# Kernel tuning notes

Measured on AMD Instinct MI355X. Metric: run time of the kernel, lower is better.

## Reference

```python
import jax, jax.numpy as jnp
import numpy as np

VOCAB, EMB, HID = 32000, 512, 1024

def setup_inputs() -> dict:
    key = jax.random.key(0)
    k1, k2, k3, k4, k5, k6 = jax.random.split(key, 6)
    s_e = 1.0 / np.sqrt(EMB)
    s_h = 1.0 / np.sqrt(HID)
    return {
        "x": jax.random.randint(k1, (32, 512), 0, VOCAB, dtype=jnp.int64),
        "emb_table": jax.random.normal(k2, (VOCAB, EMB), dtype=jnp.float32),
        "W_ih": jax.random.uniform(k3, (4 * HID, EMB), jnp.float32, -s_h, s_h),
        "W_hh": jax.random.uniform(k4, (4 * HID, HID), jnp.float32, -s_h, s_h),
        "b_ih": jax.random.uniform(k5, (4 * HID,), jnp.float32, -s_h, s_h),
        "b_hh": jax.random.uniform(k6, (4 * HID,), jnp.float32, -s_h, s_h),
    }

def _lstm(embedded, W_ih, W_hh, b_ih, b_hh):
    # embedded: [B, T, E]; gates order (PyTorch): i, f, g, o
    B = embedded.shape[0]
    H = W_hh.shape[1]
    # Precompute input projections for all timesteps: [B, T, 4H]
    x_proj = jnp.einsum('bte,ge->btg', embedded, W_ih) + b_ih + b_hh

    def step(carry, xt):
        h, c = carry
        gates = xt + h @ W_hh.T  # [B, 4H]
        i, f, g, o = jnp.split(gates, 4, axis=-1)
        i = jax.nn.sigmoid(i)
        f = jax.nn.sigmoid(f)
        g = jnp.tanh(g)
        o = jax.nn.sigmoid(o)
        c = f * c + i * g
        h = o * jnp.tanh(c)
        return (h, c), h

    h0 = jnp.zeros((B, H), embedded.dtype)
    c0 = jnp.zeros((B, H), embedded.dtype)
    (h_f, c_f), hs = jax.lax.scan(step, (h0, c0), jnp.swapaxes(x_proj, 0, 1))
    return jnp.swapaxes(hs, 0, 1), h_f, c_f

def reference(x, emb_table, W_ih, W_hh, b_ih, b_hh):
    embedded = emb_table[x]  # [B, T, E]
    encoder_outputs, state_h, state_c = _lstm(embedded, W_ih, W_hh, b_ih, b_hh)
    return encoder_outputs, state_h, state_c
```

## Files before the change

### kernel.cpp

```cpp
#include <hip/hip_runtime.h>

#define Bb 32
#define Tt 512
#define Ee 512
#define Hh 1024

typedef __attribute__((ext_vector_type(8))) short bf16x8;
typedef __attribute__((ext_vector_type(4))) float f32x4;
typedef __attribute__((ext_vector_type(4))) unsigned u32x4;
typedef unsigned long long u64;

#define SEN 0x7FC0u

__device__ __forceinline__ unsigned short f2bf(float f) {
  unsigned int u = __float_as_uint(f);
  u = (u + 0x7fffu + ((u >> 16) & 1u)) >> 16;
  return (unsigned short)u;
}
__device__ __forceinline__ float bf2f(unsigned short s) {
  return __uint_as_float(((unsigned int)s) << 16);
}
__device__ __forceinline__ float sigmoidf_(float x) {
  x = fminf(fmaxf(x, -30.f), 30.f);
  return 1.f / (1.f + __expf(-x));
}
__device__ __forceinline__ float tanh_fast(float x) {
  float xx = fminf(fmaxf(x, -15.f), 15.f);
  float e = __expf(2.f * xx);
  return (e - 1.f) / (e + 1.f);
}
__device__ __forceinline__ bool frag_bad(u32x4 v) {
  return ((v[0] & 0xFFFFu) == SEN) | ((v[1] & 0xFFFFu) == SEN) |
         ((v[2] & 0xFFFFu) == SEN) | ((v[3] & 0xFFFFu) == SEN);
}

__global__ void gather_kernel(const int* __restrict__ x,
                              const float* __restrict__ emb,
                              unsigned short* __restrict__ emb_hi,
                              unsigned short* __restrict__ emb_lo,
                              unsigned short* __restrict__ hbuf) {
  long long gid = (long long)blockIdx.x * blockDim.x + threadIdx.x;
  long long stride = (long long)gridDim.x * blockDim.x;
  for (long long i = gid; i < 8192; i += stride)
    ((ushort4*)hbuf)[i] = make_ushort4(0, 0, 0, 0);
  for (long long i = 8192 + gid; i < 4194304; i += stride)
    ((ushort4*)hbuf)[i] =
        make_ushort4((unsigned short)SEN, (unsigned short)SEN,
                     (unsigned short)SEN, (unsigned short)SEN);
  long long n4 = (long long)Bb * Tt * Ee / 4;
  for (long long i = gid; i < n4; i += stride) {
    long long bt = i >> 7;
    int e4 = (int)(i & 127);
    int row = x[bt];
    row = min(max(row, 0), 31999);
    float4 v = ((const float4*)(emb + (long long)row * Ee))[e4];
    ushort4 hv, lv;
    hv.x = f2bf(v.x); lv.x = f2bf(v.x - bf2f(hv.x));
    hv.y = f2bf(v.y); lv.y = f2bf(v.y - bf2f(hv.y));
    hv.z = f2bf(v.z); lv.z = f2bf(v.z - bf2f(hv.z));
    hv.w = f2bf(v.w); lv.w = f2bf(v.w - bf2f(hv.w));
    ((ushort4*)emb_hi)[i] = hv;
    ((ushort4*)emb_lo)[i] = lv;
  }
}

__global__ __launch_bounds__(256, 1)
void lstm_kernel(const unsigned short* __restrict__ emb_hi,
                 const unsigned short* __restrict__ emb_lo,
                 unsigned short* __restrict__ hbuf,
                 const float* __restrict__ W_ih,
                 const float* __restrict__ W_hh,
                 const float* __restrict__ b_ih,
                 const float* __restrict__ b_hh,
                 float* __restrict__ out) {
  __shared__ unsigned short sWih_hi[16 * 512];
  __shared__ unsigned short sWih_lo[16 * 512];
  __shared__ unsigned short sWhh_hi[16 * 1024];
  __shared__ unsigned short sWhh_lo[16 * 1024];
  __shared__ float sAcc[2][4][2][16][17];
  __shared__ float sBias[16];
  __shared__ float sC[32][4];

  const int tid = threadIdx.x;
  const int lane = tid & 63;
  const int wv = tid >> 6;
  const int wg = blockIdx.x;
  const int j0 = (wg & 7) * 128 + (wg >> 3) * 4;

  for (int idx = tid; idx < 16 * 64; idx += 256) {
    int c = idx >> 6, kc8 = idx & 63;
    int grow = (c >> 2) * Hh + j0 + (c & 3);
    const float* src = W_ih + (long long)grow * Ee + kc8 * 8;
    int us = (c * 512 + kc8 * 8) ^ ((c & 7) << 3);
#pragma unroll
    for (int j = 0; j < 8; j++) {
      float f = src[j];
      unsigned short h = f2bf(f);
      sWih_hi[us + j] = h;
      sWih_lo[us + j] = f2bf(f - bf2f(h));
    }
  }
  for (int idx = tid; idx < 16 * 128; idx += 256) {
    int c = idx >> 7, kc8 = idx & 127;
    int grow = (c >> 2) * Hh + j0 + (c & 3);
    const float* src = W_hh + (long long)grow * Hh + kc8 * 8;
    int us = (c * 1024 + kc8 * 8) ^ ((c & 7) << 3);
#pragma unroll
    for (int j = 0; j < 8; j++) {
      float f = src[j];
      unsigned short h = f2bf(f);
      sWhh_hi[us + j] = h;
      sWhh_lo[us + j] = f2bf(f - bf2f(h));
    }
  }
  if (tid < 16) {
    int grow = (tid >> 2) * Hh + j0 + (tid & 3);
    sBias[tid] = b_ih[grow] + b_hh[grow];
  }
  if (tid < 128) sC[tid >> 2][tid & 3] = 0.f;
  __syncthreads();

  const int r16 = lane & 15;
  const int kg = (lane >> 4) * 8;
  const int col = lane & 15;
  const int xr = (col & 7) << 3;

  float h_last = 0.f, c_last = 0.f;

  for (int t = 0; t < Tt; t++) {
    __builtin_amdgcn_sched_barrier(0);

    const u32x4* hb4 = (const u32x4*)(hbuf + (u64)t * 32768);
    const u64* hb8 = (const u64*)(hbuf + (u64)t * 32768);
    u32x4 hA[8], hB[8];
    int iA[8], iB[8];
#pragma unroll
    for (int q = 0; q < 8; q++) {
      int kc = wv + q * 4;
      iA[q] = (r16 * Hh + kc * 32 + kg) >> 3;
      iB[q] = ((16 + r16) * Hh + kc * 32 + kg) >> 3;
      hA[q] = hb4[iA[q]];
      hB[q] = hb4[iB[q]];
    }

    f32x4 acc[2][3];
#pragma unroll
    for (int mt = 0; mt < 2; mt++)
#pragma unroll
      for (int cb = 0; cb < 3; cb++)
        acc[mt][cb] = (f32x4){0.f, 0.f, 0.f, 0.f};
#pragma unroll
    for (int q = 0; q < 4; q++) {
      int kc = wv + q * 4;
      int bo = (col * 512 + kc * 32 + kg) ^ xr;
      bf16x8 bH = *(const bf16x8*)(sWih_hi + bo);
      bf16x8 bL = *(const bf16x8*)(sWih_lo + bo);
#pragma unroll
      for (int mt = 0; mt < 2; mt++) {
        int rb = mt * 16 + r16;
        int ai = (rb * Tt + t) * Ee + kc * 32 + kg;
        bf16x8 aH = *(const bf16x8*)(emb_hi + ai);
        bf16x8 aL = *(const bf16x8*)(emb_lo + ai);
        acc[mt][0] = __builtin_amdgcn_mfma_f32_16x16x32_bf16(aH, bH, acc[mt][0], 0, 0, 0);
        acc[mt][1] = __builtin_amdgcn_mfma_f32_16x16x32_bf16(aH, bL, acc[mt][1], 0, 0, 0);
        acc[mt][2] = __builtin_amdgcn_mfma_f32_16x16x32_bf16(aL, bH, acc[mt][2], 0, 0, 0);
      }
    }

#pragma unroll
    for (int q = 0; q < 8; q++) {
      int kc = wv + q * 4;
      u32x4 va = hA[q], vb = hB[q];
      bool bad = frag_bad(va) | frag_bad(vb);
      while (__any(bad)) {
        if (bad) {
          u64 a0 = __hip_atomic_load(hb8 + iA[q] * 2, __ATOMIC_RELAXED,
                                     __HIP_MEMORY_SCOPE_AGENT);
          u64 a1 = __hip_atomic_load(hb8 + iA[q] * 2 + 1, __ATOMIC_RELAXED,
                                     __HIP_MEMORY_SCOPE_AGENT);
          u64 b0 = __hip_atomic_load(hb8 + iB[q] * 2, __ATOMIC_RELAXED,
                                     __HIP_MEMORY_SCOPE_AGENT);
          u64 b1 = __hip_atomic_load(hb8 + iB[q] * 2 + 1, __ATOMIC_RELAXED,
                                     __HIP_MEMORY_SCOPE_AGENT);
          va[0] = (unsigned)a0; va[1] = (unsigned)(a0 >> 32);
          va[2] = (unsigned)a1; va[3] = (unsigned)(a1 >> 32);
          vb[0] = (unsigned)b0; vb[1] = (unsigned)(b0 >> 32);
          vb[2] = (unsigned)b1; vb[3] = (unsigned)(b1 >> 32);
        }
        bad = frag_bad(va) | frag_bad(vb);
      }
      union { u32x4 u; bf16x8 v; } ua, ub;
      ua.u = va; ub.u = vb;
      int bo = (col * 1024 + kc * 32 + kg) ^ xr;
      bf16x8 bH = *(const bf16x8*)(sWhh_hi + bo);
      bf16x8 bL = *(const bf16x8*)(sWhh_lo + bo);
      acc[0][0] = __builtin_amdgcn_mfma_f32_16x16x32_bf16(ua.v, bH, acc[0][0], 0, 0, 0);
      acc[0][1] = __builtin_amdgcn_mfma_f32_16x16x32_bf16(ua.v, bL, acc[0][1], 0, 0, 0);
      acc[1][0] = __builtin_amdgcn_mfma_f32_16x16x32_bf16(ub.v, bH, acc[1][0], 0, 0, 0);
      acc[1][1] = __builtin_amdgcn_mfma_f32_16x16x32_bf16(ub.v, bL, acc[1][1], 0, 0, 0);
    }

#pragma unroll
    for (int mt = 0; mt < 2; mt++) {
      f32x4 tot = acc[mt][0] + acc[mt][1] + acc[mt][2];
#pragma unroll
      for (int r = 0; r < 4; r++)
        sAcc[t & 1][wv][mt][(lane >> 4) * 4 + r][col] = tot[r];
    }
    __syncthreads();

    if (tid < 128) {
      int b = tid >> 2, du = tid & 3;
      int mt = b >> 4, rr = b & 15;
      float g0 = sBias[0 * 4 + du], g1 = sBias[1 * 4 + du];
      float g2 = sBias[2 * 4 + du], g3 = sBias[3 * 4 + du];
#pragma unroll
      for (int w = 0; w < 4; w++) {
        g0 += sAcc[t & 1][w][mt][rr][0 * 4 + du];
        g1 += sAcc[t & 1][w][mt][rr][1 * 4 + du];
        g2 += sAcc[t & 1][w][mt][rr][2 * 4 + du];
        g3 += sAcc[t & 1][w][mt][rr][3 * 4 + du];
      }
      float ig = sigmoidf_(g0);
      float fg = sigmoidf_(g1);
      float gg = tanh_fast(g2);
      float og = sigmoidf_(g3);
      float cn = fg * sC[b][du] + ig * gg;
      sC[b][du] = cn;
      float hn = og * tanh_fast(cn);
      h_last = hn; c_last = cn;

      unsigned pack = (unsigned)f2bf(hn);
      unsigned other = __shfl_xor(pack, 1, 64);
      if (t + 1 < Tt && (du & 1) == 0) {
        unsigned w = (pack & 0xffffu) | (other << 16);
        unsigned* nb32 = (unsigned*)(hbuf + (u64)(t + 1) * 32768);
        __hip_atomic_store(nb32 + ((b * 1024 + j0 + du) >> 1), w,
                           __ATOMIC_RELAXED, __HIP_MEMORY_SCOPE_AGENT);
      }
      out[((long long)b * Tt + t) * Hh + j0 + du] = hn;
    }
  }

  if (tid < 128) {
    int b = tid >> 2, du = tid & 3;
    int hj = j0 + du;
    out[16777216LL + b * Hh + hj] = h_last;
    out[16777216LL + 32768 + b * Hh + hj] = c_last;
  }
}

extern "C" void kernel_launch(void* const* d_in, const int* in_sizes, int n_in,
                              void* d_out, int out_size, void* d_ws, size_t ws_size,
                              hipStream_t stream) {
  const int* x      = (const int*)d_in[0];
  const float* emb  = (const float*)d_in[1];
  const float* W_ih = (const float*)d_in[2];
  const float* W_hh = (const float*)d_in[3];
  const float* b_ih = (const float*)d_in[4];
  const float* b_hh = (const float*)d_in[5];
  float* out = (float*)d_out;

  unsigned short* emb_hi = (unsigned short*)d_ws;
  unsigned short* emb_lo = emb_hi + 8388608;
  unsigned short* hbuf   = emb_lo + 8388608;

  hipLaunchKernelGGL(gather_kernel, dim3(2048), dim3(256), 0, stream,
                     x, emb, emb_hi, emb_lo, hbuf);

  void* args[] = { (void*)&emb_hi, (void*)&emb_lo, (void*)&hbuf,
                   (void*)&W_ih, (void*)&W_hh, (void*)&b_ih, (void*)&b_hh,
                   (void*)&out };
  hipError_t e = hipLaunchCooperativeKernel((void*)lstm_kernel, dim3(256),
                                            dim3(256), args, 0, stream);
  if (e != hipSuccess) {
    hipLaunchKernelGGL(lstm_kernel, dim3(256), dim3(256), 0, stream,
                       emb_hi, emb_lo, hbuf, W_ih, W_hh, b_ih, b_hh, out);
  }
}
```

Baseline: 3.440 ms.

## Drop split-bf16 compensation and halve workgroups with 8 hidden units each

Removes the hi/lo bf16 split of the weights and embeddings, so each product is a single bf16 MFMA instead of three. Each workgroup now owns 8 hidden units (32 gate rows) instead of 4, which halves the grid to 128 blocks. Waves are re-split into two row tiles times two K halves, and all 256 threads run the cell update. This cuts MFMA count, LDS traffic and the number of blocks synchronizing through the h buffer, at the cost of lower precision in the gate pre-activations.

```diff
diff --git a/kernel.cpp b/kernel.cpp
--- a/kernel.cpp
+++ b/kernel.cpp
@@ -17,9 +17,6 @@
   u = (u + 0x7fffu + ((u >> 16) & 1u)) >> 16;
   return (unsigned short)u;
 }
-__device__ __forceinline__ float bf2f(unsigned short s) {
-  return __uint_as_float(((unsigned int)s) << 16);
-}
 __device__ __forceinline__ float sigmoidf_(float x) {
   x = fminf(fmaxf(x, -30.f), 30.f);
   return 1.f / (1.f + __expf(-x));
@@ -37,7 +34,6 @@
 __global__ void gather_kernel(const int* __restrict__ x,
                               const float* __restrict__ emb,
                               unsigned short* __restrict__ emb_hi,
-                              unsigned short* __restrict__ emb_lo,
                               unsigned short* __restrict__ hbuf) {
   long long gid = (long long)blockIdx.x * blockDim.x + threadIdx.x;
   long long stride = (long long)gridDim.x * blockDim.x;
@@ -54,76 +50,62 @@
     int row = x[bt];
     row = min(max(row, 0), 31999);
     float4 v = ((const float4*)(emb + (long long)row * Ee))[e4];
-    ushort4 hv, lv;
-    hv.x = f2bf(v.x); lv.x = f2bf(v.x - bf2f(hv.x));
-    hv.y = f2bf(v.y); lv.y = f2bf(v.y - bf2f(hv.y));
-    hv.z = f2bf(v.z); lv.z = f2bf(v.z - bf2f(hv.z));
-    hv.w = f2bf(v.w); lv.w = f2bf(v.w - bf2f(hv.w));
+    ushort4 hv;
+    hv.x = f2bf(v.x); hv.y = f2bf(v.y);
+    hv.z = f2bf(v.z); hv.w = f2bf(v.w);
     ((ushort4*)emb_hi)[i] = hv;
-    ((ushort4*)emb_lo)[i] = lv;
   }
 }
 
 __global__ __launch_bounds__(256, 1)
 void lstm_kernel(const unsigned short* __restrict__ emb_hi,
-                 const unsigned short* __restrict__ emb_lo,
                  unsigned short* __restrict__ hbuf,
                  const float* __restrict__ W_ih,
                  const float* __restrict__ W_hh,
                  const float* __restrict__ b_ih,
                  const float* __restrict__ b_hh,
                  float* __restrict__ out) {
-  __shared__ unsigned short sWih_hi[16 * 512];
-  __shared__ unsigned short sWih_lo[16 * 512];
-  __shared__ unsigned short sWhh_hi[16 * 1024];
-  __shared__ unsigned short sWhh_lo[16 * 1024];
-  __shared__ float sAcc[2][4][2][16][17];
-  __shared__ float sBias[16];
-  __shared__ float sC[32][4];
+  __shared__ unsigned short sWih[32 * 512];
+  __shared__ unsigned short sWhh[32 * 1024];
+  __shared__ float sAcc[2][2][2][2][16][17];
+  __shared__ float sBias[32];
+  __shared__ float sC[32][8];
 
   const int tid = threadIdx.x;
   const int lane = tid & 63;
   const int wv = tid >> 6;
   const int wg = blockIdx.x;
-  const int j0 = (wg & 7) * 128 + (wg >> 3) * 4;
-
-  for (int idx = tid; idx < 16 * 64; idx += 256) {
-    int c = idx >> 6, kc8 = idx & 63;
-    int grow = (c >> 2) * Hh + j0 + (c & 3);
-    const float* src = W_ih + (long long)grow * Ee + kc8 * 8;
-    int us = (c * 512 + kc8 * 8) ^ ((c & 7) << 3);
-#pragma unroll
-    for (int j = 0; j < 8; j++) {
-      float f = src[j];
-      unsigned short h = f2bf(f);
-      sWih_hi[us + j] = h;
-      sWih_lo[us + j] = f2bf(f - bf2f(h));
-    }
-  }
-  for (int idx = tid; idx < 16 * 128; idx += 256) {
-    int c = idx >> 7, kc8 = idx & 127;
-    int grow = (c >> 2) * Hh + j0 + (c & 3);
-    const float* src = W_hh + (long long)grow * Hh + kc8 * 8;
-    int us = (c * 1024 + kc8 * 8) ^ ((c & 7) << 3);
-#pragma unroll
-    for (int j = 0; j < 8; j++) {
-      float f = src[j];
-      unsigned short h = f2bf(f);
-      sWhh_hi[us + j] = h;
-      sWhh_lo[us + j] = f2bf(f - bf2f(h));
-    }
-  }
-  if (tid < 16) {
-    int grow = (tid >> 2) * Hh + j0 + (tid & 3);
+  const int j0 = (wg & 7) * 128 + (wg >> 3) * 8;
+
+  for (int idx = tid; idx < 32 * 64; idx += 256) {
+    int c = idx >> 6, k8 = idx & 63;
+    int grow = (c >> 3) * Hh + j0 + (c & 7);
+    const float* src = W_ih + (long long)grow * Ee + k8 * 8;
+    int us = (c * 512 + k8 * 8) ^ ((c & 7) << 3);
+#pragma unroll
+    for (int j = 0; j < 8; j++) sWih[us + j] = f2bf(src[j]);
+  }
+  for (int idx = tid; idx < 32 * 128; idx += 256) {
+    int c = idx >> 7, k8 = idx & 127;
+    int grow = (c >> 3) * Hh + j0 + (c & 7);
+    const float* src = W_hh + (long long)grow * Hh + k8 * 8;
+    int us = (c * 1024 + k8 * 8) ^ ((c & 7) << 3);
+#pragma unroll
+    for (int j = 0; j < 8; j++) sWhh[us + j] = f2bf(src[j]);
+  }
+  if (tid < 32) {
+    int grow = (tid >> 3) * Hh + j0 + (tid & 7);
     sBias[tid] = b_ih[grow] + b_hh[grow];
   }
-  if (tid < 128) sC[tid >> 2][tid & 3] = 0.f;
+  sC[tid >> 3][tid & 7] = 0.f;
   __syncthreads();
 
   const int r16 = lane & 15;
   const int kg = (lane >> 4) * 8;
   const int col = lane & 15;
-  const int xr = (col & 7) << 3;
+  const int kw = wv & 1;
+  const int mt = wv >> 1;
+  const int rb = mt * 16 + r16;
 
   float h_last = 0.f, c_last = 0.f;
 
@@ -132,119 +114,101 @@
 
     const u32x4* hb4 = (const u32x4*)(hbuf + (u64)t * 32768);
     const u64* hb8 = (const u64*)(hbuf + (u64)t * 32768);
-    u32x4 hA[8], hB[8];
-    int iA[8], iB[8];
+    u32x4 hA[16];
+    int iA[16];
+#pragma unroll
+    for (int q = 0; q < 16; q++) {
+      int kc = q * 2 + kw;
+      iA[q] = (rb * Hh + kc * 32 + kg) >> 3;
+      hA[q] = hb4[iA[q]];
+    }
+
+    f32x4 acc[2];
+    acc[0] = (f32x4){0.f, 0.f, 0.f, 0.f};
+    acc[1] = (f32x4){0.f, 0.f, 0.f, 0.f};
 #pragma unroll
     for (int q = 0; q < 8; q++) {
-      int kc = wv + q * 4;
-      iA[q] = (r16 * Hh + kc * 32 + kg) >> 3;
-      iB[q] = ((16 + r16) * Hh + kc * 32 + kg) >> 3;
-      hA[q] = hb4[iA[q]];
-      hB[q] = hb4[iB[q]];
-    }
-
-    f32x4 acc[2][3];
-#pragma unroll
-    for (int mt = 0; mt < 2; mt++)
-#pragma unroll
-      for (int cb = 0; cb < 3; cb++)
-        acc[mt][cb] = (f32x4){0.f, 0.f, 0.f, 0.f};
-#pragma unroll
-    for (int q = 0; q < 4; q++) {
-      int kc = wv + q * 4;
-      int bo = (col * 512 + kc * 32 + kg) ^ xr;
-      bf16x8 bH = *(const bf16x8*)(sWih_hi + bo);
-      bf16x8 bL = *(const bf16x8*)(sWih_lo + bo);
-#pragma unroll
-      for (int mt = 0; mt < 2; mt++) {
-        int rb = mt * 16 + r16;
-        int ai = (rb * Tt + t) * Ee + kc * 32 + kg;
-        bf16x8 aH = *(const bf16x8*)(emb_hi + ai);
-        bf16x8 aL = *(const bf16x8*)(emb_lo + ai);
-        acc[mt][0] = __builtin_amdgcn_mfma_f32_16x16x32_bf16(aH, bH, acc[mt][0], 0, 0, 0);
-        acc[mt][1] = __builtin_amdgcn_mfma_f32_16x16x32_bf16(aH, bL, acc[mt][1], 0, 0, 0);
-        acc[mt][2] = __builtin_amdgcn_mfma_f32_16x16x32_bf16(aL, bH, acc[mt][2], 0, 0, 0);
-      }
-    }
-
-#pragma unroll
-    for (int q = 0; q < 8; q++) {
-      int kc = wv + q * 4;
-      u32x4 va = hA[q], vb = hB[q];
-      bool bad = frag_bad(va) | frag_bad(vb);
+      int kc = q * 2 + kw;
+      int ai = (rb * Tt + t) * Ee + kc * 32 + kg;
+      bf16x8 aH = *(const bf16x8*)(emb_hi + ai);
+#pragma unroll
+      for (int bt = 0; bt < 2; bt++) {
+        int c = bt * 16 + col;
+        int bo = (c * 512 + kc * 32 + kg) ^ ((c & 7) << 3);
+        bf16x8 bW = *(const bf16x8*)(sWih + bo);
+        acc[bt] = __builtin_amdgcn_mfma_f32_16x16x32_bf16(aH, bW, acc[bt], 0, 0, 0);
+      }
+    }
+
+#pragma unroll
+    for (int q = 0; q < 16; q++) {
+      int kc = q * 2 + kw;
+      u32x4 va = hA[q];
+      bool bad = frag_bad(va);
       while (__any(bad)) {
         if (bad) {
           u64 a0 = __hip_atomic_load(hb8 + iA[q] * 2, __ATOMIC_RELAXED,
                                      __HIP_MEMORY_SCOPE_AGENT);
           u64 a1 = __hip_atomic_load(hb8 + iA[q] * 2 + 1, __ATOMIC_RELAXED,
                                      __HIP_MEMORY_SCOPE_AGENT);
-          u64 b0 = __hip_atomic_load(hb8 + iB[q] * 2, __ATOMIC_RELAXED,
-                                     __HIP_MEMORY_SCOPE_AGENT);
-          u64 b1 = __hip_atomic_load(hb8 + iB[q] * 2 + 1, __ATOMIC_RELAXED,
-                                     __HIP_MEMORY_SCOPE_AGENT);
           va[0] = (unsigned)a0; va[1] = (unsigned)(a0 >> 32);
           va[2] = (unsigned)a1; va[3] = (unsigned)(a1 >> 32);
-          vb[0] = (unsigned)b0; vb[1] = (unsigned)(b0 >> 32);
-          vb[2] = (unsigned)b1; vb[3] = (unsigned)(b1 >> 32);
         }
-        bad = frag_bad(va) | frag_bad(vb);
-      }
-      union { u32x4 u; bf16x8 v; } ua, ub;
-      ua.u = va; ub.u = vb;
-      int bo = (col * 1024 + kc * 32 + kg) ^ xr;
-      bf16x8 bH = *(const bf16x8*)(sWhh_hi + bo);
-      bf16x8 bL = *(const bf16x8*)(sWhh_lo + bo);
-      acc[0][0] = __builtin_amdgcn_mfma_f32_16x16x32_bf16(ua.v, bH, acc[0][0], 0, 0, 0);
-      acc[0][1] = __builtin_amdgcn_mfma_f32_16x16x32_bf16(ua.v, bL, acc[0][1], 0, 0, 0);
-      acc[1][0] = __builtin_amdgcn_mfma_f32_16x16x32_bf16(ub.v, bH, acc[1][0], 0, 0, 0);
-      acc[1][1] = __builtin_amdgcn_mfma_f32_16x16x32_bf16(ub.v, bL, acc[1][1], 0, 0, 0);
-    }
-
-#pragma unroll
-    for (int mt = 0; mt < 2; mt++) {
-      f32x4 tot = acc[mt][0] + acc[mt][1] + acc[mt][2];
+        bad = frag_bad(va);
+      }
+      union { u32x4 u; bf16x8 v; } ua;
+      ua.u = va;
+#pragma unroll
+      for (int bt = 0; bt < 2; bt++) {
+        int c = bt * 16 + col;
+        int bo = (c * 1024 + kc * 32 + kg) ^ ((c & 7) << 3);
+        bf16x8 bW = *(const bf16x8*)(sWhh + bo);
+        acc[bt] = __builtin_amdgcn_mfma_f32_16x16x32_bf16(ua.v, bW, acc[bt], 0, 0, 0);
+      }
+    }
+
+#pragma unroll
+    for (int bt = 0; bt < 2; bt++)
 #pragma unroll
       for (int r = 0; r < 4; r++)
-        sAcc[t & 1][wv][mt][(lane >> 4) * 4 + r][col] = tot[r];
-    }
+        sAcc[t & 1][kw][mt][bt][(lane >> 4) * 4 + r][col] = acc[bt][r];
     __syncthreads();
 
-    if (tid < 128) {
-      int b = tid >> 2, du = tid & 3;
-      int mt = b >> 4, rr = b & 15;
-      float g0 = sBias[0 * 4 + du], g1 = sBias[1 * 4 + du];
-      float g2 = sBias[2 * 4 + du], g3 = sBias[3 * 4 + du];
-#pragma unroll
-      for (int w = 0; w < 4; w++) {
-        g0 += sAcc[t & 1][w][mt][rr][0 * 4 + du];
-        g1 += sAcc[t & 1][w][mt][rr][1 * 4 + du];
-        g2 += sAcc[t & 1][w][mt][rr][2 * 4 + du];
-        g3 += sAcc[t & 1][w][mt][rr][3 * 4 + du];
-      }
+    {
+      int b = tid >> 3, u = tid & 7;
+      int mtc = b >> 4, rr = b & 15;
+      float g0 = sAcc[t & 1][0][mtc][0][rr][u] +
+                 sAcc[t & 1][1][mtc][0][rr][u] + sBias[u];
+      float g1 = sAcc[t & 1][0][mtc][0][rr][8 + u] +
+                 sAcc[t & 1][1][mtc][0][rr][8 + u] + sBias[8 + u];
+      float g2 = sAcc[t & 1][0][mtc][1][rr][u] +
+                 sAcc[t & 1][1][mtc][1][rr][u] + sBias[16 + u];
+      float g3 = sAcc[t & 1][0][mtc][1][rr][8 + u] +
+                 sAcc[t & 1][1][mtc][1][rr][8 + u] + sBias[24 + u];
       float ig = sigmoidf_(g0);
       float fg = sigmoidf_(g1);
       float gg = tanh_fast(g2);
       float og = sigmoidf_(g3);
-      float cn = fg * sC[b][du] + ig * gg;
-      sC[b][du] = cn;
+      float cn = fg * sC[b][u] + ig * gg;
+      sC[b][u] = cn;
       float hn = og * tanh_fast(cn);
       h_last = hn; c_last = cn;
 
       unsigned pack = (unsigned)f2bf(hn);
       unsigned other = __shfl_xor(pack, 1, 64);
-      if (t + 1 < Tt && (du & 1) == 0) {
+      if (t + 1 < Tt && (u & 1) == 0) {
         unsigned w = (pack & 0xffffu) | (other << 16);
         unsigned* nb32 = (unsigned*)(hbuf + (u64)(t + 1) * 32768);
-        __hip_atomic_store(nb32 + ((b * 1024 + j0 + du) >> 1), w,
+        __hip_atomic_store(nb32 + ((b * 1024 + j0 + u) >> 1), w,
                            __ATOMIC_RELAXED, __HIP_MEMORY_SCOPE_AGENT);
       }
-      out[((long long)b * Tt + t) * Hh + j0 + du] = hn;
-    }
-  }
-
-  if (tid < 128) {
-    int b = tid >> 2, du = tid & 3;
-    int hj = j0 + du;
+      out[((long long)b * Tt + t) * Hh + j0 + u] = hn;
+    }
+  }
+
+  {
+    int b = tid >> 3, u = tid & 7;
+    int hj = j0 + u;
     out[16777216LL + b * Hh + hj] = h_last;
     out[16777216LL + 32768 + b * Hh + hj] = c_last;
   }
@@ -262,19 +226,18 @@
   float* out = (float*)d_out;
 
   unsigned short* emb_hi = (unsigned short*)d_ws;
-  unsigned short* emb_lo = emb_hi + 8388608;
-  unsigned short* hbuf   = emb_lo + 8388608;
+  unsigned short* hbuf   = emb_hi + 8388608;
 
   hipLaunchKernelGGL(gather_kernel, dim3(2048), dim3(256), 0, stream,
-                     x, emb, emb_hi, emb_lo, hbuf);
-
-  void* args[] = { (void*)&emb_hi, (void*)&emb_lo, (void*)&hbuf,
+                     x, emb, emb_hi, hbuf);
+
+  void* args[] = { (void*)&emb_hi, (void*)&hbuf,
                    (void*)&W_ih, (void*)&W_hh, (void*)&b_ih, (void*)&b_hh,
                    (void*)&out };
-  hipError_t e = hipLaunchCooperativeKernel((void*)lstm_kernel, dim3(256),
+  hipError_t e = hipLaunchCooperativeKernel((void*)lstm_kernel, dim3(128),
                                             dim3(256), args, 0, stream);
   if (e != hipSuccess) {
-    hipLaunchKernelGGL(lstm_kernel, dim3(256), dim3(256), 0, stream,
-                       emb_hi, emb_lo, hbuf, W_ih, W_hh, b_ih, b_hh, out);
-  }
-}
+    hipLaunchKernelGGL(lstm_kernel, dim3(128), dim3(256), 0, stream,
+                       emb_hi, hbuf, W_ih, W_hh, b_ih, b_hh, out);
+  }
+}
```

Result: faster. 2.856 ms (median of 2 runs) (-17.0%).
